# Kernel tuning notes

Measured on AMD Instinct MI355X. Metric: run time of the kernel, lower is better.

## Reference

```python
import jax, jax.numpy as jnp
import numpy as np

DIM = 1024
IMG_H, IMG_W = 512, 1408
CROP = 224
IMAGE_ORDER = (2, 0, 1, 5, 3, 4)
B, NC, NB = 2, 6, 32


def setup_inputs():
    key = jax.random.key(0)
    ks = jax.random.split(key, 12)
    camera_imgs = jax.random.normal(ks[0], (B, NC, 3, IMG_H, IMG_W), jnp.float32)
    u = jax.random.uniform(ks[1], (B, NB, 9), dtype=jnp.float32)
    centers = jnp.stack([u[..., 0] * 45.0 + 5.0,
                         (u[..., 1] - 0.5) * 40.0,
                         (u[..., 2] - 0.5) * 4.0], -1)
    pred_boxes = jnp.concatenate([centers, u[..., 3:] * 2.0], -1)  # [B,NB,9]
    K = np.array([[500., 0., IMG_W / 2.], [0., 500., IMG_H / 2.], [0., 0., 1.]])
    R_l2c = np.array([[0., -1., 0.], [0., 0., -1.], [1., 0., 0.]])  # lidar->camera axes
    mats = np.zeros((NC, 4, 4), np.float32)
    for c in range(NC):
        yaw = 2.0 * np.pi * c / NC
        Rz = np.array([[np.cos(yaw), -np.sin(yaw), 0.], [np.sin(yaw), np.cos(yaw), 0.], [0., 0., 1.]])
        mats[c, :3, :3] = K @ R_l2c @ Rz.T
        mats[c, 3, 3] = 1.0
    lidar2image = jnp.broadcast_to(jnp.asarray(mats), (B, NC, 4, 4))
    eye4 = jnp.eye(4, dtype=jnp.float32)
    img_aug_matrix = jnp.broadcast_to(eye4, (B, NC, 4, 4))
    lidar_aug_matrix = jnp.broadcast_to(eye4, (B, 4, 4))
    momentum = jnp.float32(0.5)
    box_default_dim = jax.random.normal(ks[2], (1, DIM), jnp.float32)
    theta_w = jnp.zeros((4, 9), jnp.float32)  # zero-init as in torch code
    theta_b = jnp.array([1., 0., 0., 1.], jnp.float32)

    def cw(k, shape):
        fan = shape[1] * shape[2] * shape[3]
        return jax.random.normal(k, shape, jnp.float32) * (2.0 / fan) ** 0.5
    conv1 = cw(ks[3], (64, 3, 7, 7))
    conv2 = cw(ks[4], (256, 64, 3, 3))
    conv3 = cw(ks[5], (DIM, 256, 3, 3))
    pos_embed = jax.random.normal(ks[6], (50, DIM), jnp.float32) * 0.02
    s = DIM ** -0.5
    wq = jax.random.normal(ks[7], (DIM, DIM), jnp.float32) * s
    wk = jax.random.normal(ks[8], (DIM, DIM), jnp.float32) * s
    wv = jax.random.normal(ks[9], (DIM, DIM), jnp.float32) * s
    wo = jax.random.normal(ks[10], (DIM, DIM), jnp.float32) * s
    return dict(camera_imgs=camera_imgs, pred_boxes=pred_boxes,
                img_aug_matrix=img_aug_matrix, lidar_aug_matrix=lidar_aug_matrix,
                lidar2image=lidar2image, momentum=momentum,
                box_default_dim=box_default_dim, theta_w=theta_w, theta_b=theta_b,
                conv1=conv1, conv2=conv2, conv3=conv3, pos_embed=pos_embed,
                wq=wq, wk=wk, wv=wv, wo=wo)


def _project(pred_boxes, lidar_aug_matrix, lidar2image, img_aug_matrix):
    # returns vu [B,NC,NB,2] = (row, col) pixel coords, on_img [B,NC,NB]
    def per_b(boxes, la, l2i, aug):
        c = boxes[:, :3] - la[:3, 3]                       # [NB,3]
        c = jnp.linalg.inv(la[:3, :3]) @ c.T               # [3,NB]
        c = l2i[:, :3, :3] @ c + l2i[:, :3, 3:4]           # [NC,3,NB]
        z = jnp.clip(c[:, 2], 1e-5, 1e5)
        xy = c[:, :2] / z[:, None]
        c = jnp.concatenate([xy, z[:, None]], 1)
        c = aug[:, :3, :3] @ c + aug[:, :3, 3:4]
        uv = c[:, :2].transpose(0, 2, 1)                   # [NC,NB,2] (col,row)
        vu = uv[..., ::-1]                                 # (row,col)
        on = (vu[..., 0] < IMG_H) & (vu[..., 0] >= 0) & (vu[..., 1] < IMG_W) & (vu[..., 1] >= 0)
        return vu, on
    return jax.vmap(per_b)(pred_boxes, lidar_aug_matrix, lidar2image, img_aug_matrix)


def _base_grid(h, w):
    # torch affine_grid align_corners=False pixel-center coords
    xs = (2.0 * jnp.arange(w) + 1.0) / w - 1.0
    ys = (2.0 * jnp.arange(h) + 1.0) / h - 1.0
    gx, gy = jnp.meshgrid(xs, ys)  # [h,w]
    return jnp.stack([gx, gy, jnp.ones_like(gx)], -1)  # [h,w,3]


def _grid_sample(img, grid):
    # img [C,H,W]; grid [...,2] xy in [-1,1]; bilinear, zeros padding, align_corners=False
    C, H, W = img.shape
    ix = ((grid[..., 0] + 1.0) * W - 1.0) / 2.0
    iy = ((grid[..., 1] + 1.0) * H - 1.0) / 2.0
    x0 = jnp.floor(ix); y0 = jnp.floor(iy)
    x1 = x0 + 1.0; y1 = y0 + 1.0
    wx = ix - x0; wy = iy - y0

    def gather(xx, yy):
        xi = jnp.clip(xx, 0, W - 1).astype(jnp.int32)
        yi = jnp.clip(yy, 0, H - 1).astype(jnp.int32)
        valid = (xx >= 0) & (xx <= W - 1) & (yy >= 0) & (yy <= H - 1)
        return img[:, yi, xi] * valid.astype(img.dtype)  # [C, ...]
    v00 = gather(x0, y0); v01 = gather(x1, y0)
    v10 = gather(x0, y1); v11 = gather(x1, y1)
    return (v00 * (1 - wx) * (1 - wy) + v01 * wx * (1 - wy)
            + v10 * (1 - wx) * wy + v11 * wx * wy)  # [C, ...]


def _clip_head(x, conv1, conv2, conv3, pos_embed, wq, wk, wv, wo):
    dn = ('NCHW', 'OIHW', 'NCHW')
    h = jax.nn.relu(jax.lax.conv_general_dilated(x, conv1, (4, 4), 'SAME', dimension_numbers=dn))
    h = jax.nn.relu(jax.lax.conv_general_dilated(h, conv2, (4, 4), 'SAME', dimension_numbers=dn))
    h = jax.nn.relu(jax.lax.conv_general_dilated(h, conv3, (2, 2), 'SAME', dimension_numbers=dn))  # [M,D,7,7]
    tok = h.reshape(h.shape[0], DIM, 49).transpose(0, 2, 1)              # [M,49,D]
    tok = jnp.concatenate([tok.mean(1, keepdims=True), tok], 1) + pos_embed  # [M,50,D]
    q = tok[:, :1] @ wq
    k = tok @ wk
    v = tok @ wv
    attn = jax.nn.softmax((q @ k.transpose(0, 2, 1)) * (DIM ** -0.5), -1)
    return ((attn @ v) @ wo)[:, 0]  # [M,D]


def reference(camera_imgs, pred_boxes, img_aug_matrix, lidar_aug_matrix, lidar2image,
              momentum, box_default_dim, theta_w, theta_b,
              conv1, conv2, conv3, pos_embed, wq, wk, wv, wo):
    N = B * NB
    vu, on_img = _project(pred_boxes, lidar_aug_matrix, lidar2image, img_aug_matrix)  # [B,NC,NB,2],[B,NC,NB]
    boxes_flat = pred_boxes.reshape(N, 9)
    rot = jnp.tanh(boxes_flat @ theta_w.T + theta_b).reshape(N, 2, 2)   # theta_rot MLP
    ty = vu[..., 0] / IMG_H * 2.0 - 1.0                                 # [B,NC,NB]
    tx = vu[..., 1] / IMG_W * 2.0 - 1.0
    pos = jnp.stack([tx, ty], -1).transpose(0, 2, 1, 3).reshape(N, NC, 2)
    theta = jnp.concatenate([jnp.broadcast_to(rot[:, None], (N, NC, 2, 2)),
                             pos[..., None]], -1)                        # [N,NC,2,3]
    base = _base_grid(CROP, CROP)                                        # [224,224,3]
    grids = jnp.einsum('hwk,ncjk->nchwj', base, theta)                   # [N,NC,224,224,2]
    grids = grids.reshape(B, NB, NC, CROP, CROP, 2)
    crops = []
    for b in range(B):
        for c in range(NC):
            smp = _grid_sample(camera_imgs[b, c], grids[b, :, c])        # [3,NB,224,224]
            crops.append(smp.transpose(1, 0, 2, 3))
    crops = jnp.stack(crops).reshape(B, NC, NB, 3, CROP, CROP)
    crops = crops.transpose(0, 2, 1, 3, 4, 5).reshape(N * NC, 3, CROP, CROP)
    emb = _clip_head(crops, conv1, conv2, conv3, pos_embed, wq, wk, wv, wo).reshape(N, NC, DIM)
    valid = on_img.transpose(0, 2, 1).reshape(N, NC)
    e = jnp.broadcast_to(box_default_dim, (N, DIM))
    for c in IMAGE_ORDER:  # sequential EMA over cameras, skipping off-image ones
        m = valid[:, c:c + 1]
        e = jnp.where(m, momentum * e + (1.0 - momentum) * emb[:, c], e)
    return e  # [N, DIM]
```

## Files before the change

### kernel.cpp

```cpp
#include <hip/hip_runtime.h>
#include <hip/hip_bf16.h>

#define DIMN 1024
#define IMG_H 512
#define IMG_W 1408
#define CROPN 224
#define NCAM 6
#define NBOXB 32
#define NBOX 64
#define NIMG 384

typedef __hip_bfloat16 bf16;
typedef unsigned short u16;
typedef float f32x4 __attribute__((ext_vector_type(4)));
typedef short bf16x8 __attribute__((ext_vector_type(8)));
typedef u16 u16x4 __attribute__((ext_vector_type(4)));
typedef u16 u16x8 __attribute__((ext_vector_type(8)));

__device__ __forceinline__ float b2f(bf16 x) { return __bfloat162float(x); }
__device__ __forceinline__ u16 f2us(float x) {
  bf16 h = __float2bfloat16(x);
  return *(u16*)&h;
}
__device__ __forceinline__ bf16x8 as_b(u16x8 x) {
  union { u16x8 u; bf16x8 b; } c; c.u = x; return c.b;
}

__global__ void k_w1r(const float* __restrict__ in, u16* __restrict__ out) {
  int idx = blockIdx.x * 256 + threadIdx.x;
  if (idx >= 64 * 224) return;
  int oc = idx / 224, t = idx % 224;
  int r = t >> 5, u = t & 31, kw = u >> 2, ch = u & 3;
  out[idx] = (kw < 7 && ch < 3) ? f2us(in[((oc * 3 + ch) * 7 + r) * 7 + kw]) : (u16)0;
}
__global__ void k_w2r(const float* __restrict__ in, u16* __restrict__ out) {
  int idx = blockIdx.x * 256 + threadIdx.x;
  if (idx >= 256 * 576) return;
  int oc = idx / 576, t = idx % 576;
  int rk = t >> 6, ic = t & 63, r = rk / 3, kw = rk % 3;
  out[idx] = f2us(in[((oc * 64 + ic) * 3 + r) * 3 + kw]);
}
__global__ void k_w3r(const float* __restrict__ in, u16* __restrict__ out) {
  int idx = blockIdx.x * 256 + threadIdx.x;
  if (idx >= 1024 * 2304) return;
  int oc = idx / 2304, t = idx % 2304;
  int rk = t >> 8, ic = t & 255, r = rk / 3, kw = rk % 3;
  u16 v = f2us(in[((oc * 256 + ic) * 3 + r) * 3 + kw]);
  int ocb = oc >> 4, mm = oc & 15, kb = t >> 3, kj = t & 7;
  out[(((size_t)ocb * 288 + kb) * 16 + mm) * 8 + kj] = v;
}
__global__ void k_transpose_t(const float* __restrict__ w, float* __restrict__ wt) {
  __shared__ float tile[32][33];
  int x = blockIdx.x * 32 + threadIdx.x;
  for (int j = threadIdx.y; j < 32; j += 8)
    tile[j][threadIdx.x] = w[(size_t)(blockIdx.y * 32 + j) * 1024 + x];
  __syncthreads();
  int x2 = blockIdx.y * 32 + threadIdx.x;
  for (int j = threadIdx.y; j < 32; j += 8)
    wt[(size_t)(blockIdx.x * 32 + j) * 1024 + x2] = tile[threadIdx.x][j];
}

__global__ void k_proj(const float* __restrict__ boxes, const float* __restrict__ la_m,
                       const float* __restrict__ l2i, const float* __restrict__ aug,
                       const float* __restrict__ tw, const float* __restrict__ tb,
                       float* __restrict__ theta_out, int* __restrict__ valid_out) {
  int t = threadIdx.x;
  if (t >= NIMG) return;
  int n = t / NCAM, cam = t % NCAM;
  int b = n / NBOXB, nb = n % NBOXB;

  float la[4][4];
  for (int r = 0; r < 4; r++)
    for (int c = 0; c < 4; c++) la[r][c] = la_m[b * 16 + r * 4 + c];
  float a00=la[0][0],a01=la[0][1],a02=la[0][2];
  float a10=la[1][0],a11=la[1][1],a12=la[1][2];
  float a20=la[2][0],a21=la[2][1],a22=la[2][2];
  float c00 =  a11*a22 - a12*a21;
  float c01 = -(a10*a22 - a12*a20);
  float c02 =  a10*a21 - a11*a20;
  float det = a00*c00 + a01*c01 + a02*c02;
  float id = 1.0f / det;
  float inv[3][3];
  inv[0][0] = c00*id;                 inv[0][1] = -(a01*a22-a02*a21)*id;  inv[0][2] =  (a01*a12-a02*a11)*id;
  inv[1][0] = c01*id;                 inv[1][1] =  (a00*a22-a02*a20)*id;  inv[1][2] = -(a00*a12-a02*a10)*id;
  inv[2][0] = c02*id;                 inv[2][1] = -(a00*a21-a01*a20)*id;  inv[2][2] =  (a00*a11-a01*a10)*id;

  float bx[9];
  for (int i = 0; i < 9; i++) bx[i] = boxes[(b * NBOXB + nb) * 9 + i];
  float c0[3] = { bx[0]-la[0][3], bx[1]-la[1][3], bx[2]-la[2][3] };
  float c1[3];
  for (int r = 0; r < 3; r++) c1[r] = inv[r][0]*c0[0] + inv[r][1]*c0[1] + inv[r][2]*c0[2];

  const float* M = l2i + (size_t)(b * NCAM + cam) * 16;
  float p[3];
  for (int r = 0; r < 3; r++)
    p[r] = M[r*4+0]*c1[0] + M[r*4+1]*c1[1] + M[r*4+2]*c1[2] + M[r*4+3];
  float z = fminf(fmaxf(p[2], 1e-5f), 100000.0f);
  float x = p[0] / z, y = p[1] / z;
  const float* A = aug + (size_t)(b * NCAM + cam) * 16;
  float u = A[0]*x + A[1]*y + A[2]*z + A[3];
  float v = A[4]*x + A[5]*y + A[6]*z + A[7];

  int on = (v < (float)IMG_H) && (v >= 0.0f) && (u < (float)IMG_W) && (u >= 0.0f);
  float ty = v / (float)IMG_H * 2.0f - 1.0f;
  float tx = u / (float)IMG_W * 2.0f - 1.0f;

  float s[4];
  for (int j = 0; j < 4; j++) {
    float acc = tb[j];
    for (int i = 0; i < 9; i++) acc += tw[j * 9 + i] * bx[i];
    s[j] = tanhf(acc);
  }
  float* o = theta_out + t * 6;
  o[0] = s[0]; o[1] = s[1]; o[2] = tx;
  o[3] = s[2]; o[4] = s[3]; o[5] = ty;
  valid_out[t] = on;
}

#define HALO_PX 1356
__global__ void k_zero_halo(u16x4* __restrict__ c) {
  int t = blockIdx.x * 256 + threadIdx.x;
  int i = t / HALO_PX;
  if (i >= NIMG) return;
  int r = t % HALO_PX;
  int ph, pw;
  if (r < 684) {
    int rr = r / 228;
    ph = (rr == 0) ? 0 : (rr == 1 ? 225 : 226);
    pw = r % 228;
  } else {
    int q = r - 684;
    ph = 1 + q / 3;
    int s = q % 3;
    pw = (s == 0) ? 0 : (s == 1 ? 225 : 226);
  }
  c[(size_t)i * 228 * 228 + ph * 228 + pw] = (u16x4){0, 0, 0, 0};
}

__global__ __launch_bounds__(256) void k_sample(const float* __restrict__ imgs,
                                                const float* __restrict__ theta,
                                                u16* __restrict__ crops) {
  int idx = blockIdx.x * 256 + threadIdx.x;
  int i = idx / (CROPN * CROPN);
  int rem = idx - i * (CROPN * CROPN);
  int yy = rem / CROPN, xx = rem % CROPN;
  const float* th = theta + i * 6;
  float gx = (2.0f * xx + 1.0f) / (float)CROPN - 1.0f;
  float gy = (2.0f * yy + 1.0f) / (float)CROPN - 1.0f;
  float grid_x = th[0]*gx + th[1]*gy + th[2];
  float grid_y = th[3]*gx + th[4]*gy + th[5];
  float ix = ((grid_x + 1.0f) * (float)IMG_W - 1.0f) * 0.5f;
  float iy = ((grid_y + 1.0f) * (float)IMG_H - 1.0f) * 0.5f;
  float x0 = floorf(ix), y0 = floorf(iy);
  float wx = ix - x0, wy = iy - y0;
  int cam = i % NCAM, b = i / (NBOXB * NCAM);
  const float* base = imgs + (size_t)(b * NCAM + cam) * 3 * IMG_H * IMG_W;

  float xf[2] = { x0, x0 + 1.0f };
  float yf[2] = { y0, y0 + 1.0f };
  float wxa[2] = { 1.0f - wx, wx };
  float wya[2] = { 1.0f - wy, wy };
  int   xi[2], yi[2], vx[2], vy[2];
  for (int j = 0; j < 2; j++) {
    vx[j] = (xf[j] >= 0.0f) && (xf[j] <= (float)(IMG_W - 1));
    vy[j] = (yf[j] >= 0.0f) && (yf[j] <= (float)(IMG_H - 1));
    xi[j] = (int)fminf(fmaxf(xf[j], 0.0f), (float)(IMG_W - 1));
    yi[j] = (int)fminf(fmaxf(yf[j], 0.0f), (float)(IMG_H - 1));
  }
  float res[3];
  #pragma unroll
  for (int ch = 0; ch < 3; ch++) {
    const float* cp = base + (size_t)ch * IMG_H * IMG_W;
    float r = 0.0f;
    #pragma unroll
    for (int jy = 0; jy < 2; jy++)
      #pragma unroll
      for (int jx = 0; jx < 2; jx++) {
        float val = (vx[jx] && vy[jy]) ? cp[yi[jy] * IMG_W + xi[jx]] : 0.0f;
        r += val * wxa[jx] * wya[jy];
      }
    res[ch] = r;
  }
  u16x4 st = { f2us(res[0]), f2us(res[1]), f2us(res[2]), 0 };
  *(u16x4*)(crops + ((size_t)i * 228 * 228 + (size_t)(yy + 1) * 228 + (xx + 1)) * 4) = st;
}


__global__ __launch_bounds__(256) void k_conv1m(const u16* __restrict__ X,
                                                const u16* __restrict__ W,
                                                u16* __restrict__ out) {
  int blk = blockIdx.x;
  int i = blk / 13, nb = blk % 13;
  int tid = threadIdx.x, wv = tid >> 6, lane = tid & 63;
  int m = lane & 15, quad = lane >> 4;
  int nbase = nb * 256 + wv * 64;
  int narr[4];
  const u16* bp[4];
  #pragma unroll
  for (int nt = 0; nt < 4; nt++) {
    int n = nbase + nt * 16 + m;
    narr[nt] = n;
    int nc = n < 3136 ? n : 3135;
    int oh = nc / 56, ow = nc - oh * 56;
    bp[nt] = X + ((size_t)i * 51984 + (size_t)(oh * 4) * 228 + ow * 4 + quad * 2) * 4;
  }
  f32x4 acc[4][4];
  #pragma unroll
  for (int t = 0; t < 4; t++)
    #pragma unroll
    for (int nt = 0; nt < 4; nt++) acc[t][nt] = (f32x4){0.f, 0.f, 0.f, 0.f};

  #pragma unroll
  for (int r = 0; r < 7; r++) {
    bf16x8 a[4];
    #pragma unroll
    for (int t = 0; t < 4; t++)
      a[t] = as_b(*(const u16x8*)(W + (t * 16 + m) * 224 + r * 32 + quad * 8));
    #pragma unroll
    for (int nt = 0; nt < 4; nt++) {
      bf16x8 bfr = as_b(*(const u16x8*)(bp[nt] + r * 912));
      #pragma unroll
      for (int t = 0; t < 4; t++)
        acc[t][nt] = __builtin_amdgcn_mfma_f32_16x16x32_bf16(a[t], bfr, acc[t][nt], 0, 0, 0);
    }
  }
  #pragma unroll
  for (int nt = 0; nt < 4; nt++) {
    int n = (narr[nt] & ~15) + m;
    if (n < 3136) {
      #pragma unroll
      for (int t = 0; t < 4; t++) {
        u16x4 st;
        #pragma unroll
        for (int r4 = 0; r4 < 4; r4++) st[r4] = f2us(fmaxf(acc[t][nt][r4], 0.f));
        *(u16x4*)(out + ((size_t)i * 3136 + n) * 64 + t * 16 + quad * 4) = st;
      }
    }
  }
}

__global__ __launch_bounds__(256) void k_conv2m(const u16* __restrict__ X,
                                                const u16* __restrict__ W,
                                                u16* __restrict__ out) {
  int blk = blockIdx.x;
  int i = blk >> 2, og = blk & 3;
  int oc0 = og * 64;
  int tid = threadIdx.x, wv = tid >> 6, lane = tid & 63;
  int m = lane & 15, quad = lane >> 4;
  int narr[4];
  const u16* bp[4];
  #pragma unroll
  for (int nt = 0; nt < 4; nt++) {
    int n = wv * 64 + nt * 16 + m;
    narr[nt] = n;
    int nc = n < 196 ? n : 195;
    int oh = nc / 14, ow = nc - oh * 14;
    bp[nt] = X + ((size_t)i * 3136 + (size_t)(oh * 4) * 56 + ow * 4) * 64 + quad * 8;
  }
  f32x4 acc[4][4];
  #pragma unroll
  for (int t = 0; t < 4; t++)
    #pragma unroll
    for (int nt = 0; nt < 4; nt++) acc[t][nt] = (f32x4){0.f, 0.f, 0.f, 0.f};

  #pragma unroll
  for (int s = 0; s < 18; s++) {
    const int rk = s >> 1, r = rk / 3, kw = rk % 3;
    const int boff = ((r * 56 + kw) * 64 + (s & 1) * 32);
    bf16x8 a[4];
    #pragma unroll
    for (int t = 0; t < 4; t++)
      a[t] = as_b(*(const u16x8*)(W + (size_t)(oc0 + t * 16 + m) * 576 + s * 32 + quad * 8));
    #pragma unroll
    for (int nt = 0; nt < 4; nt++) {
      bf16x8 bfr = as_b(*(const u16x8*)(bp[nt] + boff));
      #pragma unroll
      for (int t = 0; t < 4; t++)
        acc[t][nt] = __builtin_amdgcn_mfma_f32_16x16x32_bf16(a[t], bfr, acc[t][nt], 0, 0, 0);
    }
  }
  #pragma unroll
  for (int nt = 0; nt < 4; nt++) {
    int n = narr[nt];
    if (n < 196) {
      #pragma unroll
      for (int t = 0; t < 4; t++) {
        u16x4 st;
        #pragma unroll
        for (int r4 = 0; r4 < 4; r4++) st[r4] = f2us(fmaxf(acc[t][nt][r4], 0.f));
        *(u16x4*)(out + ((size_t)i * 196 + n) * 256 + oc0 + t * 16 + quad * 4) = st;
      }
    }
  }
}

__global__ __launch_bounds__(512, 2) void k_conv3m(const u16* __restrict__ X,
                                                   const u16* __restrict__ W,
                                                   float* __restrict__ out3) {
  __shared__ u16x8 sX8[6688];
  int bid = blockIdx.x;
  int og = (bid >> 2) & 1;
  int i  = (bid >> 3) * 4 + (bid & 3);
  int tid = threadIdx.x;

  const u16* src = X + (size_t)i * (196 * 256);
  u16x8 tmp[13];
  #pragma unroll
  for (int j = 0; j < 13; j++) {
    int c = tid + j * 512;
    int cc = c < 6272 ? c : 6271;
    tmp[j] = *(const u16x8*)(src + (size_t)cc * 8);
  }
  #pragma unroll
  for (int j = 0; j < 13; j++) {
    int c = tid + j * 512;
    sX8[(c & ~31) | ((c & 31) ^ ((c >> 6) & 7))] = tmp[j];
  }
  if (tid < 32) sX8[6656 + tid] = (u16x8){0,0,0,0,0,0,0,0};
  __syncthreads();

  int wv = tid >> 6, lane = tid & 63;
  int m = lane & 15, quad = lane >> 4;
  int ocw = og * 512 + wv * 64;
  int narr[4], oh2[4], ow2[4];
  #pragma unroll
  for (int nt = 0; nt < 4; nt++) {
    int n = nt * 16 + m;
    narr[nt] = n;
    int nc = n < 49 ? n : 48;
    int oh = nc / 7, ow = nc - oh * 7;
    oh2[nt] = oh * 2; ow2[nt] = ow * 2;
  }
  f32x4 acc[4][4];
  #pragma unroll
  for (int t = 0; t < 4; t++)
    #pragma unroll
    for (int nt = 0; nt < 4; nt++) acc[t][nt] = (f32x4){0.f, 0.f, 0.f, 0.f};

  const u16* wbase = W + (size_t)(ocw >> 4) * (288 * 128) + m * 8;

  #pragma unroll
  for (int rk = 0; rk < 9; rk++) {
    const int r = rk / 3, kw = rk % 3;
    int bck[4], bxr[4];
    #pragma unroll
    for (int nt = 0; nt < 4; nt++) {
      int ih = oh2[nt] + r, iw = ow2[nt] + kw;
      bool valid = (narr[nt] < 49) && (ih < 14) && (iw < 14);
      int p = ih * 14 + iw;
      bck[nt] = valid ? p * 32 : 6656;
      bxr[nt] = valid ? ((p >> 1) & 7) : 0;
    }
    #pragma unroll
    for (int ic8 = 0; ic8 < 8; ic8++) {
      const int kblk = rk * 32 + ic8 * 4 + quad;
      bf16x8 a[4];
      #pragma unroll
      for (int t = 0; t < 4; t++)
        a[t] = as_b(*(const u16x8*)(wbase + ((size_t)t * 288 + kblk) * 128));
      const int q = ic8 * 4 + quad;
      #pragma unroll
      for (int nt = 0; nt < 4; nt++) {
        bf16x8 bfr = as_b(sX8[bck[nt] + (q ^ bxr[nt])]);
        #pragma unroll
        for (int t = 0; t < 4; t++)
          acc[t][nt] = __builtin_amdgcn_mfma_f32_16x16x32_bf16(a[t], bfr, acc[t][nt], 0, 0, 0);
      }
    }
  }
  #pragma unroll
  for (int nt = 0; nt < 4; nt++) {
    int n = narr[nt];
    if (n < 49) {
      #pragma unroll
      for (int t = 0; t < 4; t++) {
        f32x4 o;
        #pragma unroll
        for (int r4 = 0; r4 < 4; r4++) o[r4] = fmaxf(acc[t][nt][r4], 0.f);
        *(f32x4*)(out3 + ((size_t)i * 49 + n) * DIMN + ocw + t * 16 + quad * 4) = o;
      }
    }
  }
}

__global__ __launch_bounds__(256) void k_tok(const float* __restrict__ h,
                                             const float* __restrict__ pos,
                                             float* __restrict__ tok) {
  int blk = blockIdx.x;
  int i = blk / 50, t = blk % 50;
  int d = threadIdx.x * 4;
  float4 val;
  if (t == 0) {
    float sx = 0, sy = 0, sz = 0, sw = 0;
    for (int p = 0; p < 49; p++) {
      float4 v = *(const float4*)(h + ((size_t)i * 49 + p) * DIMN + d);
      sx += v.x; sy += v.y; sz += v.z; sw += v.w;
    }
    const float inv49 = 1.0f / 49.0f;
    val.x = sx * inv49; val.y = sy * inv49; val.z = sz * inv49; val.w = sw * inv49;
  } else {
    val = *(const float4*)(h + ((size_t)i * 49 + (t - 1)) * DIMN + d);
  }
  float4 pe = *(const float4*)(pos + (size_t)t * DIMN + d);
  float4 o; o.x = val.x + pe.x; o.y = val.y + pe.y; o.z = val.z + pe.z; o.w = val.w + pe.w;
  *(float4*)(tok + ((size_t)i * 50 + t) * DIMN + d) = o;
}

__global__ __launch_bounds__(256) void k_matvec2(const float* __restrict__ vecs, int vstride,
                                                 const float* __restrict__ M,
                                                 float* __restrict__ out) {
  __shared__ float s_v[4][DIMN];
  int i0 = blockIdx.x * 4;
  int h = blockIdx.y;
  for (int e = threadIdx.x; e < 4 * DIMN; e += 256)
    s_v[e >> 10][e & 1023] = vecs[(size_t)(i0 + (e >> 10)) * vstride + (e & 1023)];
  __syncthreads();
  int d0 = h * 512 + threadIdx.x * 2;
  float2 acc[4] = {{0,0},{0,0},{0,0},{0,0}};
  for (int e = 0; e < DIMN; e++) {
    float2 w = *(const float2*)(M + (size_t)e * DIMN + d0);
    #pragma unroll
    for (int im = 0; im < 4; im++) {
      float x = s_v[im][e];
      acc[im].x += x * w.x; acc[im].y += x * w.y;
    }
  }
  #pragma unroll
  for (int im = 0; im < 4; im++)
    *(float2*)(out + (size_t)(i0 + im) * DIMN + d0) = acc[im];
}

__global__ __launch_bounds__(256) void k_attn(const float* __restrict__ tok,
                                              const float* __restrict__ a1,
                                              float* __restrict__ tvec) {
  __shared__ float s_a[DIMN];
  __shared__ float s_sc[50];
  __shared__ float s_at[50];
  int i = blockIdx.x;
  for (int e = threadIdx.x; e < DIMN; e += 256) s_a[e] = a1[(size_t)i * DIMN + e];
  __syncthreads();
  int wave = threadIdx.x >> 6, lane = threadIdx.x & 63;
  for (int t = wave; t < 50; t += 4) {
    const float* tr = tok + ((size_t)i * 50 + t) * DIMN;
    float p = 0.0f;
    for (int mm = 0; mm < 16; mm++) {
      int e = lane + mm * 64;
      p += tr[e] * s_a[e];
    }
    for (int off = 32; off > 0; off >>= 1) p += __shfl_down(p, off, 64);
    if (lane == 0) s_sc[t] = p * 0.03125f;
  }
  __syncthreads();
  if (threadIdx.x == 0) {
    float mx = s_sc[0];
    for (int t = 1; t < 50; t++) mx = fmaxf(mx, s_sc[t]);
    float sum = 0.0f;
    for (int t = 0; t < 50; t++) { float ex = expf(s_sc[t] - mx); s_at[t] = ex; sum += ex; }
    float inv = 1.0f / sum;
    for (int t = 0; t < 50; t++) s_at[t] *= inv;
  }
  __syncthreads();
  int d0 = threadIdx.x * 4;
  float ax = 0, ay = 0, az = 0, aw = 0;
  for (int t = 0; t < 50; t++) {
    float at = s_at[t];
    float4 tv = *(const float4*)(tok + ((size_t)i * 50 + t) * DIMN + d0);
    ax += at * tv.x; ay += at * tv.y; az += at * tv.z; aw += at * tv.w;
  }
  float4 o; o.x = ax; o.y = ay; o.z = az; o.w = aw;
  *(float4*)(tvec + (size_t)i * DIMN + d0) = o;
}

__global__ void k_final(const float* __restrict__ emb,
                        const int* __restrict__ valid,
                        const float* __restrict__ bdd,
                        const float* __restrict__ momp,
                        float* __restrict__ out) {
  int n = blockIdx.x;
  int d0 = threadIdx.x * 4;
  float mom = momp[0];
  float e[4];
  #pragma unroll
  for (int j = 0; j < 4; j++) e[j] = bdd[d0 + j];
  const int order[6] = {2, 0, 1, 5, 3, 4};
  #pragma unroll
  for (int s = 0; s < 6; s++) {
    int c = order[s];
    int i = n * NCAM + c;
    if (valid[i]) {
      const float* er = emb + (size_t)i * DIMN + d0;
      #pragma unroll
      for (int j = 0; j < 4; j++) e[j] = mom * e[j] + (1.0f - mom) * er[j];
    }
  }
  #pragma unroll
  for (int j = 0; j < 4; j++) out[(size_t)n * DIMN + d0 + j] = e[j];
}

extern "C" void kernel_launch(void* const* d_in, const int* in_sizes, int n_in,
                              void* d_out, int out_size, void* d_ws, size_t ws_size,
                              hipStream_t stream) {
  const float* in_cam = (const float*)d_in[0];
  const float* in_box = (const float*)d_in[1];
  const float* in_aug = (const float*)d_in[2];
  const float* in_la  = (const float*)d_in[3];
  const float* in_l2i = (const float*)d_in[4];
  const float* in_mom = (const float*)d_in[5];
  const float* in_bdd = (const float*)d_in[6];
  const float* in_tw  = (const float*)d_in[7];
  const float* in_tb  = (const float*)d_in[8];
  const float* in_c1  = (const float*)d_in[9];
  const float* in_c2  = (const float*)d_in[10];
  const float* in_c3  = (const float*)d_in[11];
  const float* in_pe  = (const float*)d_in[12];
  const float* in_wq  = (const float*)d_in[13];
  const float* in_wk  = (const float*)d_in[14];
  const float* in_wv  = (const float*)d_in[15];
  const float* in_wo  = (const float*)d_in[16];

  char* base = (char*)d_ws;
  size_t off = 0;
  auto carve = [&](size_t bytes) -> char* {
    char* p = base + off;
    off += (bytes + 255) & ~(size_t)255;
    return p;
  };
  float* theta   = (float*)carve((size_t)NIMG * 6 * 4);
  int*   valid   = (int*)carve((size_t)NIMG * 4);
  float* qbuf    = (float*)carve((size_t)NIMG * DIMN * 4);
  float* a1buf   = (float*)carve((size_t)NIMG * DIMN * 4);
  float* tvbuf   = (float*)carve((size_t)NIMG * DIMN * 4);
  float* ctxbuf  = (float*)carve((size_t)NIMG * DIMN * 4);
  float* embbuf  = (float*)carve((size_t)NIMG * DIMN * 4);
  float* wkT_f   = (float*)carve((size_t)DIMN * DIMN * 4);
  u16*   W1r     = (u16*)carve((size_t)64 * 224 * 2);
  u16*   W2r     = (u16*)carve((size_t)256 * 576 * 2);
  u16*   W3r     = (u16*)carve((size_t)1024 * 2304 * 2);
  u16*   c2o     = (u16*)carve((size_t)NIMG * 196 * 256 * 2);
  char*  R1      = carve((size_t)NIMG * 228 * 228 * 4 * 2);
  u16*   c1o     = (u16*)carve((size_t)NIMG * 3136 * 64 * 2);
  u16*   crops   = (u16*)R1;
  float* conv3o  = (float*)R1;
  float* tok     = (float*)(R1 + (size_t)NIMG * 49 * DIMN * 4);

  k_w1r<<<56, 256, 0, stream>>>(in_c1, W1r);
  k_w2r<<<576, 256, 0, stream>>>(in_c2, W2r);
  k_w3r<<<9216, 256, 0, stream>>>(in_c3, W3r);
  k_transpose_t<<<dim3(32, 32), dim3(32, 8), 0, stream>>>(in_wk, wkT_f);

  k_proj<<<1, 384, 0, stream>>>(in_box, in_la, in_l2i, in_aug, in_tw, in_tb, theta, valid);
  k_zero_halo<<<(NIMG * HALO_PX + 255) / 256, 256, 0, stream>>>((u16x4*)crops);
  k_sample<<<(NIMG * CROPN * CROPN) / 256, 256, 0, stream>>>(in_cam, theta, crops);
  k_conv1m<<<NIMG * 13, 256, 0, stream>>>(crops, W1r, c1o);
  k_conv2m<<<NIMG * 4, 256, 0, stream>>>(c1o, W2r, c2o);
  k_conv3m<<<768, 512, 0, stream>>>(c2o, W3r, conv3o);
  k_tok<<<NIMG * 50, 256, 0, stream>>>(conv3o, in_pe, tok);
  k_matvec2<<<dim3(96, 2), 256, 0, stream>>>(tok, 50 * DIMN, in_wq, qbuf);
  k_matvec2<<<dim3(96, 2), 256, 0, stream>>>(qbuf, DIMN, wkT_f, a1buf);
  k_attn<<<NIMG, 256, 0, stream>>>(tok, a1buf, tvbuf);
  k_matvec2<<<dim3(96, 2), 256, 0, stream>>>(tvbuf, DIMN, in_wv, ctxbuf);
  k_matvec2<<<dim3(96, 2), 256, 0, stream>>>(ctxbuf, DIMN, in_wo, embbuf);
  k_final<<<NBOX, 256, 0, stream>>>(embbuf, valid, in_bdd, in_mom, (float*)d_out);
}
```

Before: 1.056 ms.

## Stage conv1 input rows in LDS via direct global-to-LDS loads

Conv1 blocks now each cover four output rows of one image. The 19 input rows they need are staged once into shared memory with global_load_lds, and the B fragments are read from LDS instead of overlapping global loads. The conv1 weights are also repacked into an MFMA-friendly blocked layout so A-fragment loads are contiguous. In exchange the grid grows from 13 to 14 blocks per image, and each wave handles 64 columns of which only 56 are valid, so some MFMA work is wasted.

```diff
diff --git a/kernel.cpp b/kernel.cpp
--- a/kernel.cpp
+++ b/kernel.cpp
@@ -31,7 +31,8 @@
   if (idx >= 64 * 224) return;
   int oc = idx / 224, t = idx % 224;
   int r = t >> 5, u = t & 31, kw = u >> 2, ch = u & 3;
-  out[idx] = (kw < 7 && ch < 3) ? f2us(in[((oc * 3 + ch) * 7 + r) * 7 + kw]) : (u16)0;
+  u16 v = (kw < 7 && ch < 3) ? f2us(in[((oc * 3 + ch) * 7 + r) * 7 + kw]) : (u16)0;
+  out[(((oc >> 4) * 28 + (t >> 3)) * 16 + (oc & 15)) * 8 + (t & 7)] = v;
 }
 __global__ void k_w2r(const float* __restrict__ in, u16* __restrict__ out) {
   int idx = blockIdx.x * 256 + threadIdx.x;
@@ -186,24 +187,34 @@
 }
 
 
+#define C1_GROUPS 34
 __global__ __launch_bounds__(256) void k_conv1m(const u16* __restrict__ X,
                                                 const u16* __restrict__ W,
                                                 u16* __restrict__ out) {
+  __shared__ u16x8 sX[C1_GROUPS * 64];
   int blk = blockIdx.x;
-  int i = blk / 13, nb = blk % 13;
+  int i = blk / 14, rg = blk % 14;
   int tid = threadIdx.x, wv = tid >> 6, lane = tid & 63;
   int m = lane & 15, quad = lane >> 4;
-  int nbase = nb * 256 + wv * 64;
-  int narr[4];
-  const u16* bp[4];
-  #pragma unroll
-  for (int nt = 0; nt < 4; nt++) {
-    int n = nbase + nt * 16 + m;
-    narr[nt] = n;
-    int nc = n < 3136 ? n : 3135;
-    int oh = nc / 56, ow = nc - oh * 56;
-    bp[nt] = X + ((size_t)i * 51984 + (size_t)(oh * 4) * 228 + ow * 4 + quad * 2) * 4;
-  }
+
+  const u16* src = X + ((size_t)i * 51984 + (size_t)(rg * 16) * 228) * 4;
+  #pragma unroll
+  for (int j = 0; j < 9; j++) {
+    int g = wv + j * 4;
+    if (g < C1_GROUPS) {
+      int c = g * 64 + lane;
+      int cc = c < 2166 ? c : 2165;
+      __builtin_amdgcn_global_load_lds(
+          (const __attribute__((address_space(1))) void*)(src + (size_t)cc * 8),
+          (__attribute__((address_space(3))) void*)(sX + g * 64),
+          16, 0, 0);
+    }
+  }
+  __syncthreads();
+
+  int col[4];
+  #pragma unroll
+  for (int nt = 0; nt < 4; nt++) col[nt] = nt * 16 + m;
   f32x4 acc[4][4];
   #pragma unroll
   for (int t = 0; t < 4; t++)
@@ -215,19 +226,22 @@
     bf16x8 a[4];
     #pragma unroll
     for (int t = 0; t < 4; t++)
-      a[t] = as_b(*(const u16x8*)(W + (t * 16 + m) * 224 + r * 32 + quad * 8));
+      a[t] = as_b(*(const u16x8*)(W + (size_t)(((t * 28 + r * 4 + quad) * 16 + m) * 8)));
+    int lrow = wv * 4 + r;
     #pragma unroll
     for (int nt = 0; nt < 4; nt++) {
-      bf16x8 bfr = as_b(*(const u16x8*)(bp[nt] + r * 912));
+      int cl = col[nt] < 56 ? col[nt] : 55;
+      bf16x8 bfr = as_b(sX[lrow * 114 + cl * 2 + quad]);
       #pragma unroll
       for (int t = 0; t < 4; t++)
         acc[t][nt] = __builtin_amdgcn_mfma_f32_16x16x32_bf16(a[t], bfr, acc[t][nt], 0, 0, 0);
     }
   }
+  int oh = rg * 4 + wv;
   #pragma unroll
   for (int nt = 0; nt < 4; nt++) {
-    int n = (narr[nt] & ~15) + m;
-    if (n < 3136) {
+    if (col[nt] < 56) {
+      int n = oh * 56 + col[nt];
       #pragma unroll
       for (int t = 0; t < 4; t++) {
         u16x4 st;
@@ -551,7 +565,7 @@
   k_proj<<<1, 384, 0, stream>>>(in_box, in_la, in_l2i, in_aug, in_tw, in_tb, theta, valid);
   k_zero_halo<<<(NIMG * HALO_PX + 255) / 256, 256, 0, stream>>>((u16x4*)crops);
   k_sample<<<(NIMG * CROPN * CROPN) / 256, 256, 0, stream>>>(in_cam, theta, crops);
-  k_conv1m<<<NIMG * 13, 256, 0, stream>>>(crops, W1r, c1o);
+  k_conv1m<<<NIMG * 14, 256, 0, stream>>>(crops, W1r, c1o);
   k_conv2m<<<NIMG * 4, 256, 0, stream>>>(c1o, W2r, c2o);
   k_conv3m<<<768, 512, 0, stream>>>(c2o, W3r, conv3o);
   k_tok<<<NIMG * 50, 256, 0, stream>>>(conv3o, in_pe, tok);
```

New measurement: 1.009 ms. -4.5%, faster.
